# Kernel optimization log

Measured on AMD Instinct MI355X. Metric: run time of the kernel, lower is better.

## Reference

```python
import jax, jax.numpy as jnp
import numpy as np

N_NODES = 100000
N_EDGES = 6400000
N_ORDERS = 4
EPO = N_EDGES // N_ORDERS  # edges per order
K = 10


def setup_inputs() -> dict:
    key = jax.random.key(0)
    ks = jax.random.split(key, 7)
    x = jax.random.normal(ks[0], (N_NODES, K), dtype=jnp.float32)
    w_mp = jax.random.normal(ks[1], (K, 2 * K), dtype=jnp.float32) * (1.0 / np.sqrt(2 * K))
    b_mp = jax.random.normal(ks[2], (K,), dtype=jnp.float32) * 0.01
    w_out = jax.random.normal(ks[3], (K, K), dtype=jnp.float32) * (1.0 / np.sqrt(K))
    b_out = jax.random.normal(ks[4], (K,), dtype=jnp.float32) * 0.01
    edge_index = jax.random.randint(ks[5], (2, N_EDGES), 0, N_NODES, dtype=jnp.int64)
    orders = jax.random.randint(ks[6], (N_ORDERS, EPO), 0, N_EDGES, dtype=jnp.int64)
    return {"x": x, "w_mp": w_mp, "b_mp": b_mp, "w_out": w_out,
            "b_out": b_out, "edge_index": edge_index, "orders": orders}


def reference(x, w_mp, b_mp, w_out, b_out, edge_index, orders):
    n = x.shape[0]

    def step(h, order_idx):
        ei = edge_index[:, order_idx]            # [2, EPO] edges of this order
        # torch code swaps rows [1,0] before propagate, so in PyG terms:
        # source j = original row 1, target i = original row 0
        dst = ei[0]
        src = ei[1]
        x_i = h[dst]                             # [EPO, K]
        x_j = h[src]                             # [EPO, K]
        msg_in = jnp.concatenate([x_i, x_j - x_i], axis=1)   # [EPO, 2K]
        msg = msg_in @ w_mp.T + b_mp             # [EPO, K]
        aggr = jax.ops.segment_sum(msg, dst, num_segments=n)  # scatter-add
        return aggr + h, None                    # update(): aggr_out + x

    h, _ = jax.lax.scan(step, x, orders)
    return h @ w_out.T + b_out
```

## Files before the change

kernel.cpp:

```cpp
#include <hip/hip_runtime.h>

#define BLK 256
#define TILEB 4096
#define IPTB 16
#define CAPB 4608
#define MAXNBD 512
#define OVFN 65536

__global__ void k_init_h(const float* __restrict__ x, float* __restrict__ h, int n) {
    int total = n * 16;
    int gs = gridDim.x * blockDim.x;
    for (int i = blockIdx.x * blockDim.x + threadIdx.x; i < total; i += gs) {
        int row = i >> 4, col = i & 15;
        h[i] = (col < 10) ? x[row * 10 + col] : 0.0f;
    }
}

__global__ void k_pairs(const int* __restrict__ ei, int2* __restrict__ pairs, int ne) {
    int gs = gridDim.x * blockDim.x;
    for (int i = blockIdx.x * blockDim.x + threadIdx.x; i < ne; i += gs)
        pairs[i] = make_int2(ei[i], ei[(size_t)ne + i]);
}

template<bool PAIRS>
__global__ __launch_bounds__(256) void k_binD(const int* __restrict__ ei,
                                              const int2* __restrict__ pairs, int ne,
                                              const int* __restrict__ orders, int epo,
                                              int tps, int NBD,
                                              int* __restrict__ gcnt2,
                                              unsigned* __restrict__ recs2,
                                              int* __restrict__ ovf_cnt,
                                              int2* __restrict__ ovf) {
    __shared__ int bcnt[MAXNBD];
    __shared__ int gbase[MAXNBD];
    int t = threadIdx.x;
    int st = blockIdx.x / tps;
    int tb = blockIdx.x % tps;
    for (int i = t; i < NBD; i += 256) bcnt[i] = 0;
    __syncthreads();

    int base = tb * TILEB;
    const int* ord = orders + (size_t)st * epo;

    int idxs[IPTB];
    #pragma unroll
    for (int q = 0; q < IPTB; ++q) {
        int e = base + q * 256 + t;
        idxs[q] = (e < epo) ? ord[e] : -1;
    }
    int dv[IPTB], sv[IPTB];
    #pragma unroll
    for (int q = 0; q < IPTB; ++q) {
        dv[q] = 0; sv[q] = 0;
        if (idxs[q] >= 0) {
            if (PAIRS) { int2 p = pairs[idxs[q]]; dv[q] = p.x; sv[q] = p.y; }
            else       { dv[q] = ei[idxs[q]]; sv[q] = ei[(size_t)ne + idxs[q]]; }
        }
    }
    unsigned rec[IPTB]; int meta[IPTB];
    #pragma unroll
    for (int q = 0; q < IPTB; ++q) {
        meta[q] = -1; rec[q] = 0u;
        if (idxs[q] >= 0) {
            int key = dv[q] >> 8;
            int rk = atomicAdd(&bcnt[key], 1);
            rec[q] = ((unsigned)(dv[q] & 255) << 20) | (unsigned)sv[q];
            meta[q] = (key << 13) | rk;
        }
    }
    __syncthreads();
    for (int k = t; k < NBD; k += 256) {
        int c = bcnt[k];
        gbase[k] = c ? atomicAdd(&gcnt2[st * NBD + k], c) : 0;
    }
    __syncthreads();
    #pragma unroll
    for (int q = 0; q < IPTB; ++q) {
        if (meta[q] >= 0) {
            int key = meta[q] >> 13, rk = meta[q] & 8191;
            int pos = gbase[key] + rk;
            if (pos < CAPB) {
                recs2[((size_t)st * NBD + key) * CAPB + pos] = rec[q];
            } else {
                int o = atomicAdd(ovf_cnt, 1);
                if (o < OVFN) {
                    int d = key * 256 + (int)(rec[q] >> 20);
                    ovf[o] = make_int2((st << 18) | d, (int)(rec[q] & 0xFFFFFu));
                }
            }
        }
    }
}

__global__ __launch_bounds__(512) void k_agg2(const float* __restrict__ h_cur,
                                              float* __restrict__ h_next,
                                              const int* __restrict__ gcnt2_st,
                                              const unsigned* __restrict__ recs2_st,
                                              const float* __restrict__ w_mp,
                                              const float* __restrict__ b_mp, int n) {
    __shared__ unsigned srt[CAPB];
    __shared__ int cnts[256];
    __shared__ int sc[256];
    __shared__ int offs[257];
    __shared__ float part[256 * 10];
    __shared__ float Wa[100], Wb[100], Bm[10];
    int t = threadIdx.x;
    if (t < 100) {
        int k = t / 10, j = t - k * 10;
        float w1 = w_mp[k * 20 + j];
        float w2 = w_mp[k * 20 + 10 + j];
        Wa[t] = w1 - w2; Wb[t] = w2;
    }
    if (t < 10) Bm[t] = b_mp[t];
    if (t < 256) cnts[t] = 0;
    __syncthreads();

    int bkt = blockIdx.x;
    int cnt = gcnt2_st[bkt];
    if (cnt > CAPB) cnt = CAPB;
    const unsigned* strm = recs2_st + (size_t)bkt * CAPB;

    unsigned myrec[(CAPB + 511) / 512];
    int nm = 0;
    for (int r = t; r < cnt; r += 512) {
        unsigned rec = strm[r];
        myrec[nm++] = rec;
        atomicAdd(&cnts[rec >> 20], 1);
    }
    __syncthreads();

    if (t < 256) sc[t] = cnts[t];
    __syncthreads();
    for (int off = 1; off < 256; off <<= 1) {
        int v = (t < 256 && t >= off) ? sc[t - off] : 0;
        __syncthreads();
        if (t < 256) sc[t] += v;
        __syncthreads();
    }
    if (t < 256) offs[t + 1] = sc[t];
    if (t == 0) offs[0] = 0;
    __syncthreads();
    if (t < 256) cnts[t] = offs[t];
    __syncthreads();

    for (int q = 0; q < nm; ++q) {
        unsigned rec = myrec[q];
        int pos = atomicAdd(&cnts[rec >> 20], 1);
        srt[pos] = rec;
    }
    __syncthreads();

    int node = t & 255, half = t >> 8;
    int b0 = offs[node], m = offs[node + 1] - b0;
    float S[10] = {0,0,0,0,0,0,0,0,0,0};
    for (int p = b0 + half; p < b0 + m; p += 2) {
        int s = (int)(srt[p] & 0xFFFFFu);
        const float* pj = h_cur + (size_t)s * 16;
        float4 a0 = *(const float4*)(pj);
        float4 a1 = *(const float4*)(pj + 4);
        float2 a2 = *(const float2*)(pj + 8);
        S[0] += a0.x; S[1] += a0.y; S[2] += a0.z; S[3] += a0.w;
        S[4] += a1.x; S[5] += a1.y; S[6] += a1.z; S[7] += a1.w;
        S[8] += a2.x; S[9] += a2.y;
    }
    if (half == 1) {
        #pragma unroll
        for (int j = 0; j < 10; ++j) part[node * 10 + j] = S[j];
    }
    __syncthreads();
    if (half == 0) {
        int i = bkt * 256 + node;
        if (i < n) {
            #pragma unroll
            for (int j = 0; j < 10; ++j) S[j] += part[node * 10 + j];
            const float* pi = h_cur + (size_t)i * 16;
            float4 x0 = *(const float4*)(pi);
            float4 x1 = *(const float4*)(pi + 4);
            float2 x2 = *(const float2*)(pi + 8);
            float xi[10] = {x0.x, x0.y, x0.z, x0.w, x1.x, x1.y, x1.z, x1.w, x2.x, x2.y};
            float deg = (float)m;
            float o[10];
            #pragma unroll
            for (int k = 0; k < 10; ++k) {
                float ma = Bm[k];
                float mb = 0.0f;
                #pragma unroll
                for (int j = 0; j < 10; ++j) {
                    ma += Wa[k * 10 + j] * xi[j];
                    mb += Wb[k * 10 + j] * S[j];
                }
                o[k] = xi[k] + deg * ma + mb;
            }
            float* po = h_next + (size_t)i * 16;
            *(float4*)(po)     = make_float4(o[0], o[1], o[2], o[3]);
            *(float4*)(po + 4) = make_float4(o[4], o[5], o[6], o[7]);
            *(float2*)(po + 8) = make_float2(o[8], o[9]);
        }
    }
}

__global__ void k_fix(const float* __restrict__ h_cur, float* __restrict__ h_next,
                      const int* __restrict__ ovf_cnt, const int2* __restrict__ ovf,
                      const float* __restrict__ w_mp, const float* __restrict__ b_mp,
                      int st) {
    __shared__ float Wa[100], Wb[100], Bm[10];
    int t = threadIdx.x;
    if (t < 100) {
        int k = t / 10, j = t - k * 10;
        float w1 = w_mp[k * 20 + j];
        float w2 = w_mp[k * 20 + 10 + j];
        Wa[t] = w1 - w2; Wb[t] = w2;
    }
    if (t < 10) Bm[t] = b_mp[t];
    __syncthreads();
    int c = *ovf_cnt; if (c > OVFN) c = OVFN;
    int gs = gridDim.x * blockDim.x;
    for (int i = blockIdx.x * blockDim.x + t; i < c; i += gs) {
        int2 p = ovf[i];
        if ((p.x >> 18) != st) continue;
        int d = p.x & 0x3FFFF, s = p.y;
        const float* pi = h_cur + (size_t)d * 16;
        const float* pj = h_cur + (size_t)s * 16;
        float xi[10], xj[10];
        #pragma unroll
        for (int j = 0; j < 10; ++j) { xi[j] = pi[j]; xj[j] = pj[j]; }
        float* po = h_next + (size_t)d * 16;
        #pragma unroll
        for (int k = 0; k < 10; ++k) {
            float m = Bm[k];
            #pragma unroll
            for (int j = 0; j < 10; ++j) m += Wa[k * 10 + j] * xi[j] + Wb[k * 10 + j] * xj[j];
            atomicAdd(po + k, m);
        }
    }
}

__global__ void k_out(const float* __restrict__ h, const float* __restrict__ w_out,
                      const float* __restrict__ b_out, float* __restrict__ out, int n) {
    __shared__ float W[100];
    __shared__ float B[10];
    int t = threadIdx.x;
    if (t < 100) W[t] = w_out[t];
    if (t < 10)  B[t] = b_out[t];
    __syncthreads();
    int gs = gridDim.x * blockDim.x;
    for (int i = blockIdx.x * blockDim.x + t; i < n; i += gs) {
        float xi[10];
        #pragma unroll
        for (int j = 0; j < 10; ++j) xi[j] = h[(size_t)i * 16 + j];
        #pragma unroll
        for (int k = 0; k < 10; ++k) {
            float m = B[k];
            #pragma unroll
            for (int j = 0; j < 10; ++j) m += W[k * 10 + j] * xi[j];
            out[(size_t)i * 10 + k] = m;
        }
    }
}


__global__ void k_init10(const float* __restrict__ x, float* __restrict__ h, int n10) {
    int gs = gridDim.x * blockDim.x;
    for (int i = blockIdx.x * blockDim.x + threadIdx.x; i < n10; i += gs) h[i] = x[i];
}
__global__ void k_copy4(const float4* __restrict__ src, float4* __restrict__ dst, int n4) {
    int gs = gridDim.x * blockDim.x;
    for (int i = blockIdx.x * blockDim.x + threadIdx.x; i < n4; i += gs) dst[i] = src[i];
}
__global__ void k_edge_step10(const float* __restrict__ h_cur, float* __restrict__ h_next,
                              const int* __restrict__ edge_index, const int* __restrict__ order,
                              const float* __restrict__ w_mp, const float* __restrict__ b_mp,
                              int epo, int ne) {
    __shared__ float Wc[200]; __shared__ float Bc[10];
    int t = threadIdx.x;
    if (t < 200) {
        int k = t / 20, j = t - k * 20;
        float w = w_mp[t];
        Wc[t] = (j < 10) ? (w - w_mp[k * 20 + j + 10]) : w;
    }
    if (t < 10) Bc[t] = b_mp[t];
    __syncthreads();
    int gs = gridDim.x * blockDim.x;
    for (int e = blockIdx.x * blockDim.x + t; e < epo; e += gs) {
        int idx = order[e];
        int dst = edge_index[idx];
        int src = edge_index[(size_t)ne + idx];
        const float* pi = h_cur + (size_t)dst * 10;
        const float* pj = h_cur + (size_t)src * 10;
        float xi[10], xj[10];
        #pragma unroll
        for (int j = 0; j < 10; ++j) { xi[j] = pi[j]; xj[j] = pj[j]; }
        float* po = h_next + (size_t)dst * 10;
        #pragma unroll
        for (int k = 0; k < 10; ++k) {
            float m = Bc[k];
            #pragma unroll
            for (int j = 0; j < 10; ++j) m += Wc[k * 20 + j] * xi[j] + Wc[k * 20 + 10 + j] * xj[j];
            atomicAdd(po + k, m);
        }
    }
}
__global__ void k_out10(const float* __restrict__ h, const float* __restrict__ w_out,
                        const float* __restrict__ b_out, float* __restrict__ out, int n) {
    __shared__ float W[100]; __shared__ float B[10];
    int t = threadIdx.x;
    if (t < 100) W[t] = w_out[t];
    if (t < 10)  B[t] = b_out[t];
    __syncthreads();
    int gs = gridDim.x * blockDim.x;
    for (int i = blockIdx.x * blockDim.x + t; i < n; i += gs) {
        float xi[10];
        #pragma unroll
        for (int j = 0; j < 10; ++j) xi[j] = h[(size_t)i * 10 + j];
        #pragma unroll
        for (int k = 0; k < 10; ++k) {
            float m = B[k];
            #pragma unroll
            for (int j = 0; j < 10; ++j) m += W[k * 10 + j] * xi[j];
            out[(size_t)i * 10 + k] = m;
        }
    }
}


extern "C" void kernel_launch(void* const* d_in, const int* in_sizes, int n_in,
                              void* d_out, int out_size, void* d_ws, size_t ws_size,
                              hipStream_t stream) {
    const float* x      = (const float*)d_in[0];
    const float* w_mp   = (const float*)d_in[1];
    const float* b_mp   = (const float*)d_in[2];
    const float* w_out  = (const float*)d_in[3];
    const float* b_out  = (const float*)d_in[4];
    const int*   edge_i = (const int*)d_in[5];
    const int*   orders = (const int*)d_in[6];

    int n  = in_sizes[0] / 10;
    int ne = in_sizes[5] / 2;
    const int n_orders = 4;
    int epo = in_sizes[6] / n_orders;

    float* out = (float*)d_out;

    int NBD = (n + 255) >> 8;
    int tps = (epo + TILEB - 1) / TILEB;

    size_t off_hA    = 0;
    size_t off_hB    = off_hA + (size_t)n * 16;
    size_t off_recs2 = off_hB + (size_t)n * 16;
    size_t off_ovf   = off_recs2 + (size_t)4 * NBD * CAPB;
    size_t off_gcnt2 = off_ovf + (size_t)2 * OVFN;
    size_t off_cnt   = off_gcnt2 + (size_t)4 * NBD;
    size_t off_pairs = (off_cnt + 2) & ~(size_t)1;
    size_t need_base  = (off_cnt + 1) * 4;
    size_t need_pairs = (off_pairs + (size_t)2 * ne) * 4;

    bool ok = (ws_size >= need_base) && (NBD <= MAXNBD) && (n < (1 << 17));

    if (!ok) {
        float* hA = (float*)d_ws;
        float* hB = hA + (size_t)n * 10;
        int n10 = n * 10;
        hipLaunchKernelGGL(k_init10, dim3(min((n10 + BLK - 1) / BLK, 2048)), dim3(BLK), 0, stream,
                           x, hA, n10);
        int n4 = n10 / 4;
        float* cur = hA; float* nxt = hB;
        int gb_edge = min((epo + BLK - 1) / BLK, 6400);
        for (int s = 0; s < n_orders; ++s) {
            hipLaunchKernelGGL(k_copy4, dim3(min((n4 + BLK - 1) / BLK, 2048)), dim3(BLK), 0, stream,
                               (const float4*)cur, (float4*)nxt, n4);
            hipLaunchKernelGGL(k_edge_step10, dim3(gb_edge), dim3(BLK), 0, stream,
                               cur, nxt, edge_i, orders + (size_t)s * epo, w_mp, b_mp, epo, ne);
            float* t2 = cur; cur = nxt; nxt = t2;
        }
        hipLaunchKernelGGL(k_out10, dim3(min((n + BLK - 1) / BLK, 2048)), dim3(BLK), 0, stream,
                           cur, w_out, b_out, out, n);
        return;
    }

    float*    hA      = (float*)d_ws;
    float*    hB      = (float*)d_ws + off_hB;
    unsigned* recs2   = (unsigned*)d_ws + off_recs2;
    int2*     ovf     = (int2*)((int*)d_ws + off_ovf);
    int*      gcnt2   = (int*)d_ws + off_gcnt2;
    int*      ovf_cnt = (int*)d_ws + off_cnt;
    bool use_pairs = (ws_size >= need_pairs);
    int2* pairs = use_pairs ? (int2*)((int*)d_ws + off_pairs) : nullptr;

    hipMemsetAsync(gcnt2, 0, ((size_t)4 * NBD + 1) * sizeof(int), stream);

    int gb_init = min((n * 16 + BLK - 1) / BLK, 2048);
    hipLaunchKernelGGL(k_init_h, dim3(gb_init), dim3(BLK), 0, stream, x, hA, n);

    if (use_pairs) {
        int gb_p = min((ne + BLK - 1) / BLK, 4096);
        hipLaunchKernelGGL(k_pairs, dim3(gb_p), dim3(BLK), 0, stream, edge_i, pairs, ne);
        hipLaunchKernelGGL((k_binD<true>), dim3(4 * tps), dim3(256), 0, stream,
                           edge_i, pairs, ne, orders, epo, tps, NBD,
                           gcnt2, recs2, ovf_cnt, ovf);
    } else {
        hipLaunchKernelGGL((k_binD<false>), dim3(4 * tps), dim3(256), 0, stream,
                           edge_i, nullptr, ne, orders, epo, tps, NBD,
                           gcnt2, recs2, ovf_cnt, ovf);
    }

    float* cur = hA; float* nxt = hB;
    for (int s = 0; s < n_orders; ++s) {
        hipLaunchKernelGGL(k_agg2, dim3(NBD), dim3(512), 0, stream,
                           cur, nxt, gcnt2 + (size_t)s * NBD,
                           recs2 + (size_t)s * NBD * CAPB, w_mp, b_mp, n);
        hipLaunchKernelGGL(k_fix, dim3(8), dim3(256), 0, stream,
                           cur, nxt, ovf_cnt, ovf, w_mp, b_mp, s);
        float* t2 = cur; cur = nxt; nxt = t2;
    }

    hipLaunchKernelGGL(k_out, dim3(min((n + BLK - 1) / BLK, 2048)), dim3(BLK), 0, stream,
                       cur, w_out, b_out, out, n);
}
```

Before: 294.5 us.

## Two-pass binning by edge-index window to localize edge gathers; fuse output projection

Replaces the single binning pass, which gathered random edge_index entries per order, with two passes. The first buckets order indices by edge-index window of 8192. The second reads each window's edges with cache-local gathers and bins them by destination bucket per order. It also removes the pairs pre-pass and folds the final linear projection into the last aggregation and fix kernels. The cost is an extra pass over a windowed record buffer, a second overflow path, and atomics on the output in the final fix.

```diff
diff --git a/kernel.cpp b/kernel.cpp
--- a/kernel.cpp
+++ b/kernel.cpp
@@ -1,11 +1,14 @@
 #include <hip/hip_runtime.h>
 
 #define BLK 256
-#define TILEB 4096
-#define IPTB 16
 #define CAPB 4608
 #define MAXNBD 512
+#define MAXK2 2048
 #define OVFN 65536
+#define WBITS 13
+#define W1CAP 8928
+#define MAXNW 1024
+#define IPTA 32
 
 __global__ void k_init_h(const float* __restrict__ x, float* __restrict__ h, int n) {
     int total = n * 16;
@@ -16,102 +19,141 @@
     }
 }
 
-__global__ void k_pairs(const int* __restrict__ ei, int2* __restrict__ pairs, int ne) {
-    int gs = gridDim.x * blockDim.x;
-    for (int i = blockIdx.x * blockDim.x + threadIdx.x; i < ne; i += gs)
-        pairs[i] = make_int2(ei[i], ei[(size_t)ne + i]);
-}
-
-template<bool PAIRS>
-__global__ __launch_bounds__(256) void k_binD(const int* __restrict__ ei,
-                                              const int2* __restrict__ pairs, int ne,
-                                              const int* __restrict__ orders, int epo,
-                                              int tps, int NBD,
+__global__ __launch_bounds__(512) void k_win(const int* __restrict__ orders,
+                                             int total, int epo, int NW,
+                                             int* __restrict__ gcnt1,
+                                             unsigned* __restrict__ recs1,
+                                             int* __restrict__ ovf1_cnt,
+                                             unsigned* __restrict__ ovf1) {
+    __shared__ int bcnt[MAXNW];
+    __shared__ int gbase[MAXNW];
+    int t = threadIdx.x;
+    for (int i = t; i < NW; i += 512) bcnt[i] = 0;
+    __syncthreads();
+
+    size_t base = (size_t)blockIdx.x * (512 * IPTA);
+    int st0 = (int)(base / (size_t)epo);
+    size_t b1 = (size_t)(st0 + 1) * (size_t)epo;
+
+    unsigned recr[IPTA]; int rr[IPTA];
+    #pragma unroll
+    for (int q = 0; q < IPTA; ++q) {
+        size_t g = base + (size_t)q * 512 + t;
+        recr[q] = 0xFFFFFFFFu; rr[q] = 0;
+        if (g < (size_t)total) {
+            int idx = orders[g];
+            int st = (g >= b1) ? (st0 + 1) : st0;
+            recr[q] = ((unsigned)st << 23) | (unsigned)idx;
+            rr[q] = atomicAdd(&bcnt[idx >> WBITS], 1);
+        }
+    }
+    __syncthreads();
+    for (int k = t; k < NW; k += 512) {
+        int c = bcnt[k];
+        gbase[k] = c ? atomicAdd(&gcnt1[k], c) : 0;
+    }
+    __syncthreads();
+    #pragma unroll
+    for (int q = 0; q < IPTA; ++q) {
+        if (recr[q] != 0xFFFFFFFFu) {
+            int idx = (int)(recr[q] & 0x7FFFFFu);
+            int key = idx >> WBITS;
+            int pos = gbase[key] + rr[q];
+            if (pos < W1CAP)
+                __builtin_nontemporal_store(recr[q], &recs1[(size_t)key * W1CAP + pos]);
+            else {
+                int o = atomicAdd(ovf1_cnt, 1);
+                if (o < OVFN) ovf1[o] = recr[q];
+            }
+        }
+    }
+}
+
+__global__ __launch_bounds__(512) void k_bin2(const int* __restrict__ ei, int ne,
+                                              const int* __restrict__ gcnt1,
+                                              const unsigned* __restrict__ recs1,
+                                              int NW, int NBD,
                                               int* __restrict__ gcnt2,
                                               unsigned* __restrict__ recs2,
-                                              int* __restrict__ ovf_cnt,
-                                              int2* __restrict__ ovf) {
-    __shared__ int bcnt[MAXNBD];
-    __shared__ int gbase[MAXNBD];
-    int t = threadIdx.x;
-    int st = blockIdx.x / tps;
-    int tb = blockIdx.x % tps;
-    for (int i = t; i < NBD; i += 256) bcnt[i] = 0;
-    __syncthreads();
-
-    int base = tb * TILEB;
-    const int* ord = orders + (size_t)st * epo;
-
-    int idxs[IPTB];
-    #pragma unroll
-    for (int q = 0; q < IPTB; ++q) {
-        int e = base + q * 256 + t;
-        idxs[q] = (e < epo) ? ord[e] : -1;
-    }
-    int dv[IPTB], sv[IPTB];
-    #pragma unroll
-    for (int q = 0; q < IPTB; ++q) {
-        dv[q] = 0; sv[q] = 0;
-        if (idxs[q] >= 0) {
-            if (PAIRS) { int2 p = pairs[idxs[q]]; dv[q] = p.x; sv[q] = p.y; }
-            else       { dv[q] = ei[idxs[q]]; sv[q] = ei[(size_t)ne + idxs[q]]; }
-        }
-    }
-    unsigned rec[IPTB]; int meta[IPTB];
-    #pragma unroll
-    for (int q = 0; q < IPTB; ++q) {
-        meta[q] = -1; rec[q] = 0u;
-        if (idxs[q] >= 0) {
-            int key = dv[q] >> 8;
-            int rk = atomicAdd(&bcnt[key], 1);
-            rec[q] = ((unsigned)(dv[q] & 255) << 20) | (unsigned)sv[q];
-            meta[q] = (key << 13) | rk;
-        }
-    }
-    __syncthreads();
-    for (int k = t; k < NBD; k += 256) {
-        int c = bcnt[k];
-        gbase[k] = c ? atomicAdd(&gcnt2[st * NBD + k], c) : 0;
-    }
-    __syncthreads();
-    #pragma unroll
-    for (int q = 0; q < IPTB; ++q) {
-        if (meta[q] >= 0) {
-            int key = meta[q] >> 13, rk = meta[q] & 8191;
-            int pos = gbase[key] + rk;
-            if (pos < CAPB) {
-                recs2[((size_t)st * NBD + key) * CAPB + pos] = rec[q];
-            } else {
-                int o = atomicAdd(ovf_cnt, 1);
-                if (o < OVFN) {
-                    int d = key * 256 + (int)(rec[q] >> 20);
-                    ovf[o] = make_int2((st << 18) | d, (int)(rec[q] & 0xFFFFFu));
-                }
+                                              int* __restrict__ ovf2_cnt,
+                                              int2* __restrict__ ovf2) {
+    __shared__ int cnt2[MAXK2];
+    __shared__ int cur[MAXK2];
+    int t = threadIdx.x;
+    int K2 = 4 * NBD;
+    for (int i = t; i < K2; i += 512) cnt2[i] = 0;
+    __syncthreads();
+
+    int w0 = blockIdx.x * 2;
+    for (int wi = 0; wi < 2; ++wi) {
+        int w = w0 + wi;
+        if (w >= NW) break;
+        int c = gcnt1[w]; if (c > W1CAP) c = W1CAP;
+        const unsigned* strm = recs1 + (size_t)w * W1CAP;
+        for (int r = t; r < c; r += 512) {
+            unsigned rec = strm[r];
+            int idx = (int)(rec & 0x7FFFFFu);
+            int st  = (int)(rec >> 23);
+            int d = ei[idx];
+            atomicAdd(&cnt2[st * NBD + (d >> 8)], 1);
+        }
+    }
+    __syncthreads();
+    for (int k = t; k < K2; k += 512) {
+        int c = cnt2[k];
+        cur[k] = c ? atomicAdd(&gcnt2[k], c) : 0;
+    }
+    __syncthreads();
+    for (int wi = 0; wi < 2; ++wi) {
+        int w = w0 + wi;
+        if (w >= NW) break;
+        int c = gcnt1[w]; if (c > W1CAP) c = W1CAP;
+        const unsigned* strm = recs1 + (size_t)w * W1CAP;
+        for (int r = t; r < c; r += 512) {
+            unsigned rec = strm[r];
+            int idx = (int)(rec & 0x7FFFFFu);
+            int st  = (int)(rec >> 23);
+            int d = ei[idx];
+            int s = ei[(size_t)ne + idx];
+            int key = st * NBD + (d >> 8);
+            int pos = atomicAdd(&cur[key], 1);
+            unsigned r2 = ((unsigned)(d & 255) << 20) | (unsigned)s;
+            if (pos < CAPB)
+                __builtin_nontemporal_store(r2, &recs2[(size_t)key * CAPB + pos]);
+            else {
+                int o = atomicAdd(ovf2_cnt, 1);
+                if (o < OVFN) ovf2[o] = make_int2((st << 18) | d, s);
             }
         }
     }
 }
 
+template<bool FINAL>
 __global__ __launch_bounds__(512) void k_agg2(const float* __restrict__ h_cur,
                                               float* __restrict__ h_next,
                                               const int* __restrict__ gcnt2_st,
                                               const unsigned* __restrict__ recs2_st,
                                               const float* __restrict__ w_mp,
-                                              const float* __restrict__ b_mp, int n) {
+                                              const float* __restrict__ b_mp,
+                                              const float* __restrict__ w_out,
+                                              const float* __restrict__ b_out,
+                                              float* __restrict__ out, int n) {
     __shared__ unsigned srt[CAPB];
     __shared__ int cnts[256];
     __shared__ int sc[256];
     __shared__ int offs[257];
     __shared__ float part[256 * 10];
     __shared__ float Wa[100], Wb[100], Bm[10];
+    __shared__ float Wo[100], Bo[10];
     int t = threadIdx.x;
     if (t < 100) {
         int k = t / 10, j = t - k * 10;
         float w1 = w_mp[k * 20 + j];
         float w2 = w_mp[k * 20 + 10 + j];
         Wa[t] = w1 - w2; Wb[t] = w2;
-    }
-    if (t < 10) Bm[t] = b_mp[t];
+        if (FINAL) Wo[t] = w_out[t];
+    }
+    if (t < 10) { Bm[t] = b_mp[t]; if (FINAL) Bo[t] = b_out[t]; }
     if (t < 256) cnts[t] = 0;
     __syncthreads();
 
@@ -191,16 +233,35 @@
                 }
                 o[k] = xi[k] + deg * ma + mb;
             }
-            float* po = h_next + (size_t)i * 16;
-            *(float4*)(po)     = make_float4(o[0], o[1], o[2], o[3]);
-            *(float4*)(po + 4) = make_float4(o[4], o[5], o[6], o[7]);
-            *(float2*)(po + 8) = make_float2(o[8], o[9]);
+            if (FINAL) {
+                float q2[10];
+                #pragma unroll
+                for (int k = 0; k < 10; ++k) {
+                    float m2 = Bo[k];
+                    #pragma unroll
+                    for (int j = 0; j < 10; ++j) m2 += Wo[k * 10 + j] * o[j];
+                    q2[k] = m2;
+                }
+                float* po = out + (size_t)i * 10;
+                *(float2*)(po)     = make_float2(q2[0], q2[1]);
+                *(float2*)(po + 2) = make_float2(q2[2], q2[3]);
+                *(float2*)(po + 4) = make_float2(q2[4], q2[5]);
+                *(float2*)(po + 6) = make_float2(q2[6], q2[7]);
+                *(float2*)(po + 8) = make_float2(q2[8], q2[9]);
+            } else {
+                float* po = h_next + (size_t)i * 16;
+                *(float4*)(po)     = make_float4(o[0], o[1], o[2], o[3]);
+                *(float4*)(po + 4) = make_float4(o[4], o[5], o[6], o[7]);
+                *(float2*)(po + 8) = make_float2(o[8], o[9]);
+            }
         }
     }
 }
 
 __global__ void k_fix(const float* __restrict__ h_cur, float* __restrict__ h_next,
-                      const int* __restrict__ ovf_cnt, const int2* __restrict__ ovf,
+                      const int* __restrict__ ei, int ne,
+                      const int* __restrict__ ovf1_cnt, const unsigned* __restrict__ ovf1,
+                      const int* __restrict__ ovf2_cnt, const int2* __restrict__ ovf2,
                       const float* __restrict__ w_mp, const float* __restrict__ b_mp,
                       int st) {
     __shared__ float Wa[100], Wb[100], Bm[10];
@@ -213,12 +274,21 @@
     }
     if (t < 10) Bm[t] = b_mp[t];
     __syncthreads();
-    int c = *ovf_cnt; if (c > OVFN) c = OVFN;
-    int gs = gridDim.x * blockDim.x;
-    for (int i = blockIdx.x * blockDim.x + t; i < c; i += gs) {
-        int2 p = ovf[i];
-        if ((p.x >> 18) != st) continue;
-        int d = p.x & 0x3FFFF, s = p.y;
+    int c1 = *ovf1_cnt; if (c1 > OVFN) c1 = OVFN;
+    int c2 = *ovf2_cnt; if (c2 > OVFN) c2 = OVFN;
+    int gs = gridDim.x * blockDim.x;
+    for (int i = blockIdx.x * blockDim.x + t; i < c1 + c2; i += gs) {
+        int d, s;
+        if (i < c1) {
+            unsigned v = ovf1[i];
+            if ((int)(v >> 23) != st) continue;
+            int idx = (int)(v & 0x7FFFFFu);
+            d = ei[idx]; s = ei[(size_t)ne + idx];
+        } else {
+            int2 p = ovf2[i - c1];
+            if ((p.x >> 18) != st) continue;
+            d = p.x & 0x3FFFF; s = p.y;
+        }
         const float* pi = h_cur + (size_t)d * 16;
         const float* pj = h_cur + (size_t)s * 16;
         float xi[10], xj[10];
@@ -235,25 +305,58 @@
     }
 }
 
-__global__ void k_out(const float* __restrict__ h, const float* __restrict__ w_out,
-                      const float* __restrict__ b_out, float* __restrict__ out, int n) {
-    __shared__ float W[100];
-    __shared__ float B[10];
-    int t = threadIdx.x;
-    if (t < 100) W[t] = w_out[t];
-    if (t < 10)  B[t] = b_out[t];
-    __syncthreads();
-    int gs = gridDim.x * blockDim.x;
-    for (int i = blockIdx.x * blockDim.x + t; i < n; i += gs) {
-        float xi[10];
-        #pragma unroll
-        for (int j = 0; j < 10; ++j) xi[j] = h[(size_t)i * 16 + j];
+__global__ void k_fix_final(const float* __restrict__ h_cur, float* __restrict__ out,
+                            const int* __restrict__ ei, int ne,
+                            const int* __restrict__ ovf1_cnt, const unsigned* __restrict__ ovf1,
+                            const int* __restrict__ ovf2_cnt, const int2* __restrict__ ovf2,
+                            const float* __restrict__ w_mp, const float* __restrict__ b_mp,
+                            const float* __restrict__ w_out, int st) {
+    __shared__ float Wa[100], Wb[100], Bm[10], Wo[100];
+    int t = threadIdx.x;
+    if (t < 100) {
+        int k = t / 10, j = t - k * 10;
+        float w1 = w_mp[k * 20 + j];
+        float w2 = w_mp[k * 20 + 10 + j];
+        Wa[t] = w1 - w2; Wb[t] = w2;
+        Wo[t] = w_out[t];
+    }
+    if (t < 10) Bm[t] = b_mp[t];
+    __syncthreads();
+    int c1 = *ovf1_cnt; if (c1 > OVFN) c1 = OVFN;
+    int c2 = *ovf2_cnt; if (c2 > OVFN) c2 = OVFN;
+    int gs = gridDim.x * blockDim.x;
+    for (int i = blockIdx.x * blockDim.x + t; i < c1 + c2; i += gs) {
+        int d, s;
+        if (i < c1) {
+            unsigned v = ovf1[i];
+            if ((int)(v >> 23) != st) continue;
+            int idx = (int)(v & 0x7FFFFFu);
+            d = ei[idx]; s = ei[(size_t)ne + idx];
+        } else {
+            int2 p = ovf2[i - c1];
+            if ((p.x >> 18) != st) continue;
+            d = p.x & 0x3FFFF; s = p.y;
+        }
+        const float* pi = h_cur + (size_t)d * 16;
+        const float* pj = h_cur + (size_t)s * 16;
+        float xi[10], xj[10];
+        #pragma unroll
+        for (int j = 0; j < 10; ++j) { xi[j] = pi[j]; xj[j] = pj[j]; }
+        float dm[10];
         #pragma unroll
         for (int k = 0; k < 10; ++k) {
-            float m = B[k];
-            #pragma unroll
-            for (int j = 0; j < 10; ++j) m += W[k * 10 + j] * xi[j];
-            out[(size_t)i * 10 + k] = m;
+            float m = Bm[k];
+            #pragma unroll
+            for (int j = 0; j < 10; ++j) m += Wa[k * 10 + j] * xi[j] + Wb[k * 10 + j] * xj[j];
+            dm[k] = m;
+        }
+        float* po = out + (size_t)d * 10;
+        #pragma unroll
+        for (int q = 0; q < 10; ++q) {
+            float m = 0.0f;
+            #pragma unroll
+            for (int k = 0; k < 10; ++k) m += Wo[q * 10 + k] * dm[k];
+            atomicAdd(po + q, m);
         }
     }
 }
@@ -338,23 +441,26 @@
     int ne = in_sizes[5] / 2;
     const int n_orders = 4;
     int epo = in_sizes[6] / n_orders;
+    int total = n_orders * epo;
 
     float* out = (float*)d_out;
 
     int NBD = (n + 255) >> 8;
-    int tps = (epo + TILEB - 1) / TILEB;
+    int NW  = (ne + (1 << WBITS) - 1) >> WBITS;
 
     size_t off_hA    = 0;
     size_t off_hB    = off_hA + (size_t)n * 16;
-    size_t off_recs2 = off_hB + (size_t)n * 16;
-    size_t off_ovf   = off_recs2 + (size_t)4 * NBD * CAPB;
-    size_t off_gcnt2 = off_ovf + (size_t)2 * OVFN;
-    size_t off_cnt   = off_gcnt2 + (size_t)4 * NBD;
-    size_t off_pairs = (off_cnt + 2) & ~(size_t)1;
-    size_t need_base  = (off_cnt + 1) * 4;
-    size_t need_pairs = (off_pairs + (size_t)2 * ne) * 4;
-
-    bool ok = (ws_size >= need_base) && (NBD <= MAXNBD) && (n < (1 << 17));
+    size_t off_recs1 = off_hB + (size_t)n * 16;
+    size_t off_recs2 = off_recs1 + (size_t)NW * W1CAP;
+    size_t off_ovf2  = off_recs2 + (size_t)4 * NBD * CAPB;
+    size_t off_ovf1  = off_ovf2 + (size_t)2 * OVFN;
+    size_t off_gcnt1 = off_ovf1 + OVFN;
+    size_t off_gcnt2 = off_gcnt1 + NW;
+    size_t off_cnts  = off_gcnt2 + (size_t)4 * NBD;
+    size_t need      = (off_cnts + 2) * 4;
+
+    bool ok = (ws_size >= need) && (NW <= MAXNW) && (NBD <= MAXNBD) &&
+              (4 * NBD <= MAXK2) && (ne <= (1 << 23)) && (n < (1 << 17));
 
     if (!ok) {
         float* hA = (float*)d_ws;
@@ -379,40 +485,50 @@
 
     float*    hA      = (float*)d_ws;
     float*    hB      = (float*)d_ws + off_hB;
+    unsigned* recs1   = (unsigned*)d_ws + off_recs1;
     unsigned* recs2   = (unsigned*)d_ws + off_recs2;
-    int2*     ovf     = (int2*)((int*)d_ws + off_ovf);
+    int2*     ovf2    = (int2*)((int*)d_ws + off_ovf2);
+    unsigned* ovf1    = (unsigned*)d_ws + off_ovf1;
+    int*      gcnt1   = (int*)d_ws + off_gcnt1;
     int*      gcnt2   = (int*)d_ws + off_gcnt2;
-    int*      ovf_cnt = (int*)d_ws + off_cnt;
-    bool use_pairs = (ws_size >= need_pairs);
-    int2* pairs = use_pairs ? (int2*)((int*)d_ws + off_pairs) : nullptr;
-
-    hipMemsetAsync(gcnt2, 0, ((size_t)4 * NBD + 1) * sizeof(int), stream);
+    int*      ovfcnts = (int*)d_ws + off_cnts;
+
+    hipMemsetAsync(gcnt1, 0, ((size_t)NW + (size_t)4 * NBD + 2) * sizeof(int), stream);
 
     int gb_init = min((n * 16 + BLK - 1) / BLK, 2048);
     hipLaunchKernelGGL(k_init_h, dim3(gb_init), dim3(BLK), 0, stream, x, hA, n);
 
-    if (use_pairs) {
-        int gb_p = min((ne + BLK - 1) / BLK, 4096);
-        hipLaunchKernelGGL(k_pairs, dim3(gb_p), dim3(BLK), 0, stream, edge_i, pairs, ne);
-        hipLaunchKernelGGL((k_binD<true>), dim3(4 * tps), dim3(256), 0, stream,
-                           edge_i, pairs, ne, orders, epo, tps, NBD,
-                           gcnt2, recs2, ovf_cnt, ovf);
-    } else {
-        hipLaunchKernelGGL((k_binD<false>), dim3(4 * tps), dim3(256), 0, stream,
-                           edge_i, nullptr, ne, orders, epo, tps, NBD,
-                           gcnt2, recs2, ovf_cnt, ovf);
-    }
+    int gbA = (total + 512 * IPTA - 1) / (512 * IPTA);
+    hipLaunchKernelGGL(k_win, dim3(gbA), dim3(512), 0, stream,
+                       orders, total, epo, NW, gcnt1, recs1, ovfcnts + 0, ovf1);
+
+    int gbB = (NW + 1) / 2;
+    hipLaunchKernelGGL(k_bin2, dim3(gbB), dim3(512), 0, stream,
+                       edge_i, ne, gcnt1, recs1, NW, NBD,
+                       gcnt2, recs2, ovfcnts + 1, ovf2);
 
     float* cur = hA; float* nxt = hB;
     for (int s = 0; s < n_orders; ++s) {
-        hipLaunchKernelGGL(k_agg2, dim3(NBD), dim3(512), 0, stream,
-                           cur, nxt, gcnt2 + (size_t)s * NBD,
-                           recs2 + (size_t)s * NBD * CAPB, w_mp, b_mp, n);
-        hipLaunchKernelGGL(k_fix, dim3(8), dim3(256), 0, stream,
-                           cur, nxt, ovf_cnt, ovf, w_mp, b_mp, s);
-        float* t2 = cur; cur = nxt; nxt = t2;
-    }
-
-    hipLaunchKernelGGL(k_out, dim3(min((n + BLK - 1) / BLK, 2048)), dim3(BLK), 0, stream,
-                       cur, w_out, b_out, out, n);
-}
+        bool fin = (s == n_orders - 1);
+        if (fin) {
+            hipLaunchKernelGGL((k_agg2<true>), dim3(NBD), dim3(512), 0, stream,
+                               cur, nxt, gcnt2 + (size_t)s * NBD,
+                               recs2 + (size_t)s * NBD * CAPB, w_mp, b_mp,
+                               w_out, b_out, out, n);
+            hipLaunchKernelGGL(k_fix_final, dim3(8), dim3(256), 0, stream,
+                               cur, out, edge_i, ne,
+                               ovfcnts + 0, ovf1, ovfcnts + 1, ovf2,
+                               w_mp, b_mp, w_out, s);
+        } else {
+            hipLaunchKernelGGL((k_agg2<false>), dim3(NBD), dim3(512), 0, stream,
+                               cur, nxt, gcnt2 + (size_t)s * NBD,
+                               recs2 + (size_t)s * NBD * CAPB, w_mp, b_mp,
+                               w_out, b_out, out, n);
+            hipLaunchKernelGGL(k_fix, dim3(8), dim3(256), 0, stream,
+                               cur, nxt, edge_i, ne,
+                               ovfcnts + 0, ovf1, ovfcnts + 1, ovf2,
+                               w_mp, b_mp, s);
+            float* t2 = cur; cur = nxt; nxt = t2;
+        }
+    }
+}
```

After: 615.9 us. 2.09x slower.
